# Optimization experiments

Hardware: AMD Instinct MI355X
Metric: run time of the kernel (lower is better)

## Reference

```python
import jax, jax.numpy as jnp
import numpy as np

N = 20000
E = 320000
H = 16
C = 16
NUM_GRAPHS = 64
NEG_SLOPE = 0.2


def _gat(x, edge_index, W, a_src, a_dst, bias):
    # PyG GATConv, concat=True, shared lin for src/dst, eval mode (no dropout)
    h = (x @ W).reshape(-1, H, C)                       # [N,H,C]
    src, dst = edge_index[0], edge_index[1]
    alpha_src = jnp.sum(h * a_src, axis=-1)             # [N,H]
    alpha_dst = jnp.sum(h * a_dst, axis=-1)             # [N,H]
    alpha = alpha_src[src] + alpha_dst[dst]             # [E,H]
    alpha = jax.nn.leaky_relu(alpha, NEG_SLOPE)
    amax = jax.ops.segment_max(alpha, dst, num_segments=N)
    ex = jnp.exp(alpha - amax[dst])
    denom = jax.ops.segment_sum(ex, dst, num_segments=N)
    attn = ex / jnp.where(denom == 0, 1.0, denom)[dst]  # [E,H]
    msg = h[src] * attn[:, :, None]                     # [E,H,C]
    out = jax.ops.segment_sum(msg, dst, num_segments=N) # [N,H,C]
    return out.reshape(-1, H * C) + bias


def setup_inputs() -> dict:
    key = jax.random.key(0)
    ks = jax.random.split(key, 32)
    d = {}
    d['x'] = jax.random.normal(ks[0], (N, 20), dtype=jnp.float32)
    d['edge_index_ipv6'] = jax.random.randint(ks[1], (2, E), 0, N)
    d['edge_attr_ipv6'] = jax.random.normal(ks[2], (E, 19), dtype=jnp.float32)
    d['edge_index_tsch'] = jax.random.randint(ks[3], (2, E), 0, N)
    d['edge_attr_tsch'] = jax.random.normal(ks[4], (E, 7), dtype=jnp.float32)
    d['batch'] = jnp.sort(jax.random.randint(ks[5], (N,), 0, NUM_GRAPHS))
    s = 0.1
    d['W_i'] = jax.random.normal(ks[6], (20, H * C), dtype=jnp.float32) * s
    d['a_src_i'] = jax.random.normal(ks[7], (H, C), dtype=jnp.float32) * s
    d['a_dst_i'] = jax.random.normal(ks[8], (H, C), dtype=jnp.float32) * s
    d['b_i'] = jnp.zeros((H * C,), dtype=jnp.float32)
    d['W_t'] = jax.random.normal(ks[9], (20, H * C), dtype=jnp.float32) * s
    d['a_src_t'] = jax.random.normal(ks[10], (H, C), dtype=jnp.float32) * s
    d['a_dst_t'] = jax.random.normal(ks[11], (H, C), dtype=jnp.float32) * s
    d['b_t'] = jnp.zeros((H * C,), dtype=jnp.float32)
    d['Wf'] = jax.random.normal(ks[12], (512, 64), dtype=jnp.float32) * s
    d['bf'] = jnp.zeros((64,), dtype=jnp.float32)
    d['W1'] = jax.random.normal(ks[13], (64, 32), dtype=jnp.float32) * s
    d['b1'] = jnp.zeros((32,), dtype=jnp.float32)
    d['W2'] = jax.random.normal(ks[14], (32, 16), dtype=jnp.float32) * s
    d['b2'] = jnp.zeros((16,), dtype=jnp.float32)
    d['W3'] = jax.random.normal(ks[15], (16, 16), dtype=jnp.float32) * s
    d['b3'] = jnp.zeros((16,), dtype=jnp.float32)
    d['Wce'] = jax.random.normal(ks[16], (16, 3), dtype=jnp.float32) * s
    d['bce'] = jnp.zeros((3,), dtype=jnp.float32)
    d['Wcv'] = jax.random.normal(ks[17], (16, 3), dtype=jnp.float32) * s
    d['bcv'] = jnp.zeros((3,), dtype=jnp.float32)
    return d


def reference(x, edge_index_ipv6, edge_attr_ipv6, edge_index_tsch, edge_attr_tsch,
              batch, W_i, a_src_i, a_dst_i, b_i, W_t, a_src_t, a_dst_t, b_t,
              Wf, bf, W1, b1, W2, b2, W3, b3, Wce, bce, Wcv, bcv):
    # edge_attr_* are ignored by GATConv (edge_dim=None in PyG), as in original
    n_ipv6 = _gat(x, edge_index_ipv6, W_i, a_src_i, a_dst_i, b_i)
    n_tsch = _gat(x, edge_index_tsch, W_t, a_src_t, a_dst_t, b_t)
    h = jnp.concatenate([n_ipv6, n_tsch], axis=-1)      # [N,512]
    h = jax.nn.relu(h @ Wf + bf)
    h = jax.nn.relu(h @ W1 + b1)
    h = jax.nn.relu(h @ W2 + b2)
    h = jax.nn.relu(h @ W3 + b3)                        # [N,16]
    ssum = jax.ops.segment_sum(h, batch, num_segments=NUM_GRAPHS)
    cnt = jax.ops.segment_sum(jnp.ones((h.shape[0], 1), h.dtype), batch,
                              num_segments=NUM_GRAPHS)
    g = ssum / jnp.where(cnt == 0, 1.0, cnt)            # [G,16]
    out_event = g @ Wce + bce
    out_env = g @ Wcv + bcv
    return out_event, out_env
```

## Files before the change

### kernel.cpp

```cpp
#include <hip/hip_runtime.h>
#include <math.h>

#define N_NODES 20000
#define N_EDGES 320000
#define NG 64
#define NEG 0.2f
#define NCHUNK ((N_NODES + 255) / 256)
#define FLAGBIT (1 << 30)

typedef __attribute__((ext_vector_type(8))) short bf16x8;
typedef __attribute__((ext_vector_type(4))) float f32x4;

__device__ __forceinline__ unsigned short f2bf(float f) {
  unsigned int u = __float_as_uint(f);
  return (unsigned short)((u + 0x7fffu + ((u >> 16) & 1u)) >> 16);
}

__global__ __launch_bounds__(256) void k_prep(
    const float* __restrict__ W_i, const float* __restrict__ as_i, const float* __restrict__ ad_i,
    const float* __restrict__ W_t, const float* __restrict__ as_t, const float* __restrict__ ad_t,
    const float* __restrict__ Wf, const float* __restrict__ bf,
    const float* __restrict__ b_i, const float* __restrict__ b_t,
    float* __restrict__ wsall, unsigned short* __restrict__ wbigfrag,
    float* __restrict__ bfold,
    int* __restrict__ fill_i, int* __restrict__ fill_t,
    float* __restrict__ gsum, int* __restrict__ gcnt, int* __restrict__ aggs) {
  __shared__ float bred[4][64];
  int idx = blockIdx.x * 256 + threadIdx.x;
  if (idx < 1280) {
    int k = idx >> 6, c = idx & 63;
    int set = c >> 5, role = (c >> 4) & 1, h = c & 15;
    const float* W = set ? W_t : W_i;
    const float* a = set ? (role ? ad_t : as_t) : (role ? ad_i : as_i);
    float v = 0.f;
#pragma unroll
    for (int j = 0; j < 16; ++j) v = fmaf(W[k * 256 + h * 16 + j], a[h * 16 + j], v);
    wsall[idx] = v;
    return;
  }
  idx -= 1280;
  if (idx < 49152) {
    int ct = idx / 12288, rem = idx % 12288;
    int lane = (rem >> 3) & 63, j = rem & 7, ks = rem >> 9;
    int k = ks * 32 + ((lane >> 4) << 3) + j;
    int nc = ct * 16 + (lane & 15);
    float v = 0.f;
    int g = (k >= 384) ? 1 : 0;
    int r = k - g * 384;
    int h = r / 24, c = r - h * 24;
    if (c < 20) {
      const float* W = g ? W_t : W_i;
      const float* wr = W + c * 256 + (h << 4);
      const float* wf = Wf + ((g << 8) + (h << 4)) * 64 + nc;
#pragma unroll
      for (int m = 0; m < 16; ++m) v = fmaf(wr[m], wf[m * 64], v);
    }
    wbigfrag[idx] = f2bf(v);
    return;
  }
  idx -= 49152;
  if (idx < 256) {
    int t = threadIdx.x, wv = t >> 6, j = t & 63;
    float p = 0.f;
    int i0 = wv * 128;
#pragma unroll 4
    for (int i = i0; i < i0 + 128; ++i) {
      float b = (i < 256) ? b_i[i] : b_t[i - 256];
      p = fmaf(b, Wf[i * 64 + j], p);
    }
    bred[wv][j] = p;
    __syncthreads();
    if (wv == 0) bfold[j] = bred[0][j] + bred[1][j] + bred[2][j] + bred[3][j] + bf[j];
    return;
  }
  idx -= 256;
  if (idx < N_NODES) { fill_i[idx] = 0; return; }
  idx -= N_NODES;
  if (idx < N_NODES) { fill_t[idx] = 0; return; }
  idx -= N_NODES;
  if (idx < NG * 16) { gsum[idx] = 0.f; return; }
  idx -= NG * 16;
  if (idx < NG) { gcnt[idx] = 0; return; }
  idx -= NG;
  if (idx < 256) aggs[idx] = 0;
}

__global__ __launch_bounds__(256) void k_alpha(
    const float* __restrict__ x, const float* __restrict__ wsall,
    float* __restrict__ xpad,
    float* __restrict__ asrc0, float* __restrict__ adst0,
    float* __restrict__ asrc1, float* __restrict__ adst1) {
  int t = threadIdx.x;
  int n0 = blockIdx.x * 16;
  __shared__ float xs[16][20];
  __shared__ float ws[20][64];
  for (int i = t; i < 16 * 20; i += 256) {
    int nd = i / 20, k = i % 20;
    xs[nd][k] = x[(n0 + nd) * 20 + k];
  }
  for (int i = t; i < 1280; i += 256) ws[i >> 6][i & 63] = wsall[i];
  __syncthreads();
  for (int i = t; i < 512; i += 256) {
    int nd = i >> 5, j = i & 31;
    xpad[(size_t)(n0 + nd) * 32 + j] = (j < 20) ? xs[nd][j] : 0.f;
  }
#pragma unroll
  for (int i = 0; i < 4; ++i) {
    int wi = i * 256 + t;
    int nd = wi >> 6, c = wi & 63;
    float v = 0.f;
#pragma unroll
    for (int k = 0; k < 20; ++k) v = fmaf(xs[nd][k], ws[k][c], v);
    int n = n0 + nd, h = c & 15;
    float* arr = (c >> 5) ? ((c >> 4) & 1 ? adst1 : asrc1)
                          : ((c >> 4) & 1 ? adst0 : asrc0);
    arr[n * 16 + h] = v;
  }
}

__global__ void k_hist(const int* __restrict__ ei0, const int* __restrict__ ei1,
                       int* __restrict__ cnt0, int* __restrict__ cnt1) {
  int e = blockIdx.x * blockDim.x + threadIdx.x;
  if (e >= N_EDGES) return;
  if (blockIdx.y == 0)
    atomicAdd(&cnt0[ei0[N_EDGES + e]], 1);
  else
    atomicAdd(&cnt1[ei1[N_EDGES + e]], 1);
}

__global__ __launch_bounds__(256) void k_scan(
    int* __restrict__ fill0, int* __restrict__ fill1,
    int* __restrict__ rp0, int* __restrict__ rp1,
    int* __restrict__ aggs) {
  int chunk = blockIdx.x, set = blockIdx.y;
  int* fill = set ? fill1 : fill0;
  int* rp = set ? rp1 : rp0;
  int t = threadIdx.x, lane = t & 63, wv = t >> 6;
  int i = chunk * 256 + t;
  int v = (i < N_NODES) ? fill[i] : 0;
  int s = v;
#pragma unroll
  for (int d = 1; d < 64; d <<= 1) {
    int o = __shfl_up(s, d);
    if (lane >= d) s += o;
  }
  __shared__ int wsum[4];
  if (lane == 63) wsum[wv] = s;
  __syncthreads();
  int pre = 0;
#pragma unroll
  for (int j = 0; j < 4; ++j)
    if (j < wv) pre += wsum[j];
  s += pre;
  int agg = wsum[0] + wsum[1] + wsum[2] + wsum[3];
  if (t == 0)
    __hip_atomic_store(&aggs[set * 128 + chunk], agg | FLAGBIT,
                       __ATOMIC_RELEASE, __HIP_MEMORY_SCOPE_AGENT);
  __shared__ int reds[256];
  int part = 0;
  for (int j = t; j < chunk; j += 256) {
    int a;
    do {
      a = __hip_atomic_load(&aggs[set * 128 + j], __ATOMIC_ACQUIRE,
                            __HIP_MEMORY_SCOPE_AGENT);
    } while (!(a & FLAGBIT));
    part += a & (FLAGBIT - 1);
  }
  reds[t] = part;
  __syncthreads();
  for (int st = 128; st > 0; st >>= 1) {
    if (t < st) reds[t] += reds[t + st];
    __syncthreads();
  }
  int carry = reds[0];
  int excl = carry + s - v;
  if (i < N_NODES) {
    rp[i] = excl;
    fill[i] = excl;
    if (i == N_NODES - 1) rp[N_NODES] = excl + v;
  }
}

__global__ void k_scatter(const int* __restrict__ ei0, const int* __restrict__ ei1,
                          int* __restrict__ fill0, int* __restrict__ fill1,
                          unsigned short* __restrict__ srcs0,
                          unsigned short* __restrict__ srcs1) {
  int e = blockIdx.x * blockDim.x + threadIdx.x;
  if (e >= N_EDGES) return;
  const int* ei = blockIdx.y ? ei1 : ei0;
  int* fill = blockIdx.y ? fill1 : fill0;
  unsigned short* srcs = blockIdx.y ? srcs1 : srcs0;
  int d = ei[N_EDGES + e];
  int pos = atomicAdd(&fill[d], 1);
  srcs[pos] = (unsigned short)ei[e];
}

__global__ __launch_bounds__(256) void k_gat(
    const float* __restrict__ xpad,
    const float* __restrict__ asrc0, const float* __restrict__ adst0,
    const float* __restrict__ asrc1, const float* __restrict__ adst1,
    const int* __restrict__ rp0, const unsigned short* __restrict__ srcs0,
    const int* __restrict__ rp1, const unsigned short* __restrict__ srcs1,
    unsigned short* __restrict__ xagg) {
  __shared__ float xsh[4][16][36];
  __shared__ float lath[4][16][16];
  int w4 = threadIdx.x >> 6, lane = threadIdx.x & 63;
  int n = blockIdx.x * 2 + (w4 >> 1);
  int g = w4 & 1;
  int h16 = lane & 15, e4 = lane >> 4;
  int eid = lane & 15, slot = lane >> 4;
  float (*xs)[36] = xsh[w4];
  float (*la)[16] = lath[w4];
  const float* asrc = g ? asrc1 : asrc0;
  const float* adst = g ? adst1 : adst0;
  const int* rp = g ? rp1 : rp0;
  const unsigned short* srcs = g ? srcs1 : srcs0;
  int k0 = rp[n], k1 = rp[n + 1];
  float4 adn4 = *(const float4*)&adst[n * 16 + slot * 4];
  float lacc = 0.f;
  float xa[8];
#pragma unroll
  for (int j = 0; j < 8; ++j) xa[j] = 0.f;
  if (k1 > k0) {
    int nbat = (k1 - k0 + 15) >> 4;
    int sb = (int)srcs[min(k0 + eid, k1 - 1)];
    float4 xv0 = *(const float4*)&xpad[(size_t)sb * 32 + slot * 8];
    float4 xv1 = *(const float4*)&xpad[(size_t)sb * 32 + slot * 8 + 4];
    float4 av4 = *(const float4*)&asrc[(size_t)sb * 16 + slot * 4];
    int sbN = 0;
    if (nbat > 1) sbN = (int)srcs[min(k0 + 16 + eid, k1 - 1)];
    for (int bb = 0; bb < nbat; ++bb) {
      float4 xv0N = {0.f,0.f,0.f,0.f}, xv1N = xv0N, av4N = xv0N;
      int sbNN = 0;
      if (bb + 1 < nbat) {
        xv0N = *(const float4*)&xpad[(size_t)sbN * 32 + slot * 8];
        xv1N = *(const float4*)&xpad[(size_t)sbN * 32 + slot * 8 + 4];
        av4N = *(const float4*)&asrc[(size_t)sbN * 16 + slot * 4];
      }
      if (bb + 2 < nbat)
        sbNN = (int)srcs[min(k0 + (bb + 2) * 16 + eid, k1 - 1)];
      bool val = (k0 + bb * 16 + eid) < k1;
      float4 ex4;
      {
        float a;
        a = av4.x + adn4.x; a = a >= 0.f ? a : NEG * a; ex4.x = val ? __expf(a) : 0.f;
        a = av4.y + adn4.y; a = a >= 0.f ? a : NEG * a; ex4.y = val ? __expf(a) : 0.f;
        a = av4.z + adn4.z; a = a >= 0.f ? a : NEG * a; ex4.z = val ? __expf(a) : 0.f;
        a = av4.w + adn4.w; a = a >= 0.f ? a : NEG * a; ex4.w = val ? __expf(a) : 0.f;
      }
      *(float4*)&xs[eid][slot * 8] = xv0;
      *(float4*)&xs[eid][slot * 8 + 4] = xv1;
      *(float4*)&la[eid][slot * 4] = ex4;
#pragma unroll
      for (int e = 0; e < 16; ++e) {
        float w = la[e][h16];
        lacc += w;
        float4 x0 = *(const float4*)&xs[e][e4 * 8];
        float4 x1 = *(const float4*)&xs[e][e4 * 8 + 4];
        xa[0] = fmaf(w, x0.x, xa[0]); xa[1] = fmaf(w, x0.y, xa[1]);
        xa[2] = fmaf(w, x0.z, xa[2]); xa[3] = fmaf(w, x0.w, xa[3]);
        xa[4] = fmaf(w, x1.x, xa[4]); xa[5] = fmaf(w, x1.y, xa[5]);
        xa[6] = fmaf(w, x1.z, xa[6]); xa[7] = fmaf(w, x1.w, xa[7]);
      }
      xv0 = xv0N; xv1 = xv1N; av4 = av4N; sb = sbN; sbN = sbNN;
    }
  }
  float invl = lacc > 0.f ? 1.f / lacc : 0.f;
  if (e4 < 3) {
    unsigned int u[4];
#pragma unroll
    for (int q = 0; q < 4; ++q)
      u[q] = (unsigned int)f2bf(xa[2 * q] * invl) |
             ((unsigned int)f2bf(xa[2 * q + 1] * invl) << 16);
    *(uint4*)&xagg[(size_t)n * 768 + g * 384 + h16 * 24 + e4 * 8] = *(uint4*)u;
  }
}

__global__ __launch_bounds__(256) void k_mlp(
    const unsigned short* __restrict__ xagg, const unsigned short* __restrict__ wbigfrag,
    const float* __restrict__ bfold,
    const float* __restrict__ W1m, const float* __restrict__ b1v,
    const float* __restrict__ W2m, const float* __restrict__ b2v,
    const float* __restrict__ W3m, const float* __restrict__ b3v,
    const int* __restrict__ batch,
    float* __restrict__ gsum, int* __restrict__ gcnt) {
  int t = threadIdx.x, w = t >> 6, lane = t & 63;
  int n0 = blockIdx.x * 16;
  __shared__ float o1[16][68];
  __shared__ float o2[16][36];
  __shared__ float o3[16][20];
  __shared__ float o4[16][17];
  __shared__ int bs[16];
  if (t < 16) bs[t] = batch[n0 + t];

  {
    int m = lane & 15, kb = lane >> 4;
    const unsigned short* aptr = xagg + (size_t)(n0 + m) * 768 + kb * 8;
    const unsigned short* bbase = wbigfrag + (size_t)w * 12288 + lane * 8;
    f32x4 acc = {0.f, 0.f, 0.f, 0.f};
#pragma unroll 6
    for (int ks = 0; ks < 24; ++ks) {
      bf16x8 af = *(const bf16x8*)(aptr + ks * 32);
      bf16x8 bfr = *(const bf16x8*)(bbase + (size_t)ks * 512);
      acc = __builtin_amdgcn_mfma_f32_16x16x32_bf16(af, bfr, acc, 0, 0, 0);
    }
    int col = lane & 15, rg = lane >> 4;
#pragma unroll
    for (int r = 0; r < 4; ++r) {
      int row = rg * 4 + r;
      o1[row][w * 16 + col] = fmaxf(acc[r] + bfold[w * 16 + col], 0.f);
    }
  }
  __syncthreads();
  int nd = t >> 4, js = t & 15;
  {
    float a0 = b1v[js], a1 = b1v[js + 16];
#pragma unroll 8
    for (int k = 0; k < 64; ++k) {
      float hv = o1[nd][k];
      a0 = fmaf(hv, W1m[k * 32 + js], a0);
      a1 = fmaf(hv, W1m[k * 32 + js + 16], a1);
    }
    o2[nd][js] = fmaxf(a0, 0.f);
    o2[nd][js + 16] = fmaxf(a1, 0.f);
  }
  __syncthreads();
  {
    float a = b2v[js];
#pragma unroll
    for (int k = 0; k < 32; ++k) a = fmaf(o2[nd][k], W2m[k * 16 + js], a);
    o3[nd][js] = fmaxf(a, 0.f);
  }
  __syncthreads();
  {
    float a = b3v[js];
#pragma unroll
    for (int k = 0; k < 16; ++k) a = fmaf(o3[nd][k], W3m[k * 16 + js], a);
    o4[nd][js] = fmaxf(a, 0.f);
  }
  __syncthreads();
  if (t < 128) {
    int s = t >> 4, jx = t & 15;
    int b = bs[0] + s;
    if (b <= bs[15]) {
      float sum = 0.f; int c = 0;
#pragma unroll
      for (int ndd = 0; ndd < 16; ++ndd)
        if (bs[ndd] == b) { sum += o4[ndd][jx]; ++c; }
      if (c > 0) {
        atomicAdd(&gsum[b * 16 + jx], sum);
        if (jx == 0) atomicAdd(&gcnt[b], c);
      }
    }
  }
}

__global__ void k_head(const float* __restrict__ gsum, const int* __restrict__ gcnt,
                       const float* __restrict__ Wce, const float* __restrict__ bce,
                       const float* __restrict__ Wcv, const float* __restrict__ bcv,
                       float* __restrict__ out) {
  int t = threadIdx.x;
  if (t >= 384) return;
  int half = t / 192, idx = t % 192;
  int b = idx / 3, r = idx % 3;
  float cnt = (float)gcnt[b];
  float inv = cnt > 0.f ? 1.f / cnt : 1.f;
  const float* Wc = half ? Wcv : Wce;
  const float* bc = half ? bcv : bce;
  float v = bc[r];
#pragma unroll
  for (int j = 0; j < 16; ++j) v = fmaf(gsum[b * 16 + j] * inv, Wc[j * 3 + r], v);
  out[t] = v;
}

extern "C" void kernel_launch(void* const* d_in, const int* in_sizes, int n_in,
                              void* d_out, int out_size, void* d_ws, size_t ws_size,
                              hipStream_t stream) {
  const float* x = (const float*)d_in[0];
  const int* ei_i = (const int*)d_in[1];
  const int* ei_t = (const int*)d_in[3];
  const int* batch = (const int*)d_in[5];
  const float* W_i = (const float*)d_in[6];
  const float* as_i = (const float*)d_in[7];
  const float* ad_i = (const float*)d_in[8];
  const float* b_i = (const float*)d_in[9];
  const float* W_t = (const float*)d_in[10];
  const float* as_t = (const float*)d_in[11];
  const float* ad_t = (const float*)d_in[12];
  const float* b_t = (const float*)d_in[13];
  const float* Wf = (const float*)d_in[14];
  const float* bf = (const float*)d_in[15];
  const float* W1 = (const float*)d_in[16];
  const float* b1 = (const float*)d_in[17];
  const float* W2 = (const float*)d_in[18];
  const float* b2 = (const float*)d_in[19];
  const float* W3 = (const float*)d_in[20];
  const float* b3 = (const float*)d_in[21];
  const float* Wce = (const float*)d_in[22];
  const float* bce = (const float*)d_in[23];
  const float* Wcv = (const float*)d_in[24];
  const float* bcv = (const float*)d_in[25];

  char* ws = (char*)d_ws;
  size_t off = 0;
  auto take = [&](size_t bytes) {
    void* p = ws + off;
    off = (off + bytes + 255) & ~(size_t)255;
    return p;
  };
  float* xpad = (float*)take((size_t)N_NODES * 32 * 4);
  unsigned short* xagg = (unsigned short*)take((size_t)N_NODES * 768 * 2);
  float* wsall = (float*)take((size_t)1280 * 4);
  unsigned short* wbigfrag = (unsigned short*)take((size_t)49152 * 2);
  float* bfold = (float*)take((size_t)64 * 4);
  float* asrc_i = (float*)take((size_t)N_NODES * 16 * 4);
  float* adst_i = (float*)take((size_t)N_NODES * 16 * 4);
  float* asrc_t = (float*)take((size_t)N_NODES * 16 * 4);
  float* adst_t = (float*)take((size_t)N_NODES * 16 * 4);
  int* rowptr_i = (int*)take((size_t)(N_NODES + 1) * 4);
  int* rowptr_t = (int*)take((size_t)(N_NODES + 1) * 4);
  int* fill_i = (int*)take((size_t)N_NODES * 4);
  int* fill_t = (int*)take((size_t)N_NODES * 4);
  int* csums = (int*)take((size_t)2 * 128 * 4);
  unsigned short* srcs_i = (unsigned short*)take((size_t)N_EDGES * 2);
  unsigned short* srcs_t = (unsigned short*)take((size_t)N_EDGES * 2);
  float* gsum = (float*)take((size_t)NG * 16 * 4);
  int* gcnt = (int*)take((size_t)NG * 4);

  int prep_items = 1280 + 49152 + 256 + N_NODES + N_NODES + NG * 16 + NG + 256;
  k_prep<<<(prep_items + 255) / 256, 256, 0, stream>>>(
      W_i, as_i, ad_i, W_t, as_t, ad_t, Wf, bf, b_i, b_t,
      wsall, wbigfrag, bfold, fill_i, fill_t, gsum, gcnt, csums);

  k_alpha<<<N_NODES / 16, 256, 0, stream>>>(x, wsall, xpad,
                                            asrc_i, adst_i, asrc_t, adst_t);

  dim3 egrid((N_EDGES + 255) / 256, 2);
  k_hist<<<egrid, 256, 0, stream>>>(ei_i, ei_t, fill_i, fill_t);
  dim3 sgrid(NCHUNK, 2);
  k_scan<<<sgrid, 256, 0, stream>>>(fill_i, fill_t, rowptr_i, rowptr_t, csums);
  k_scatter<<<egrid, 256, 0, stream>>>(ei_i, ei_t, fill_i, fill_t, srcs_i, srcs_t);

  k_gat<<<N_NODES / 2, 256, 0, stream>>>(xpad, asrc_i, adst_i, asrc_t, adst_t,
                                         rowptr_i, srcs_i, rowptr_t, srcs_t,
                                         xagg);

  k_mlp<<<N_NODES / 16, 256, 0, stream>>>(xagg, wbigfrag, bfold,
                                          W1, b1, W2, b2, W3, b3,
                                          batch, gsum, gcnt);

  k_head<<<1, 384, 0, stream>>>(gsum, gcnt, Wce, bce, Wcv, bcv, (float*)d_out);
}
```

Before: 165.1 us.

## Use bf16 MFMA for GAT neighbor aggregation with packed channel-major layout

The per-node GAT aggregation now runs on MFMA 16x16x32 bf16 instructions instead of scalar FMA loops through LDS, processing 32 edges per step. Node features are stored as bf16 with a constant-one channel at index 20, so the softmax denominator comes out of the same matrix product. The aggregated feature layout shrinks from 768 to 640 columns per node (channel-major, no per-head padding to 24), and the folded MLP weight fragments and the k_mlp loop shrink to match. This cuts gather bandwidth and ALU work, at the cost of bf16 rounding of the attention weights and features.

```diff
diff --git a/kernel.cpp b/kernel.cpp
--- a/kernel.cpp
+++ b/kernel.cpp
@@ -14,6 +14,9 @@
 __device__ __forceinline__ unsigned short f2bf(float f) {
   unsigned int u = __float_as_uint(f);
   return (unsigned short)((u + 0x7fffu + ((u >> 16) & 1u)) >> 16);
+}
+__device__ __forceinline__ unsigned int pk2bf(float a, float b) {
+  return (unsigned int)f2bf(a) | ((unsigned int)f2bf(b) << 16);
 }
 
 __global__ __launch_bounds__(256) void k_prep(
@@ -39,18 +42,18 @@
     return;
   }
   idx -= 1280;
-  if (idx < 49152) {
-    int ct = idx / 12288, rem = idx % 12288;
+  if (idx < 40960) {
+    int ct = idx / 10240, rem = idx % 10240;
     int lane = (rem >> 3) & 63, j = rem & 7, ks = rem >> 9;
     int k = ks * 32 + ((lane >> 4) << 3) + j;
     int nc = ct * 16 + (lane & 15);
+    int g = (k >= 320) ? 1 : 0;
+    int r = k - g * 320;
+    int ch = r >> 4, h = r & 15;
     float v = 0.f;
-    int g = (k >= 384) ? 1 : 0;
-    int r = k - g * 384;
-    int h = r / 24, c = r - h * 24;
-    if (c < 20) {
+    if (ch < 20) {
       const float* W = g ? W_t : W_i;
-      const float* wr = W + c * 256 + (h << 4);
+      const float* wr = W + ch * 256 + (h << 4);
       const float* wf = Wf + ((g << 8) + (h << 4)) * 64 + nc;
 #pragma unroll
       for (int m = 0; m < 16; ++m) v = fmaf(wr[m], wf[m * 64], v);
@@ -58,7 +61,7 @@
     wbigfrag[idx] = f2bf(v);
     return;
   }
-  idx -= 49152;
+  idx -= 40960;
   if (idx < 256) {
     int t = threadIdx.x, wv = t >> 6, j = t & 63;
     float p = 0.f;
@@ -87,7 +90,7 @@
 
 __global__ __launch_bounds__(256) void k_alpha(
     const float* __restrict__ x, const float* __restrict__ wsall,
-    float* __restrict__ xpad,
+    unsigned short* __restrict__ xpadbf,
     float* __restrict__ asrc0, float* __restrict__ adst0,
     float* __restrict__ asrc1, float* __restrict__ adst1) {
   int t = threadIdx.x;
@@ -102,7 +105,8 @@
   __syncthreads();
   for (int i = t; i < 512; i += 256) {
     int nd = i >> 5, j = i & 31;
-    xpad[(size_t)(n0 + nd) * 32 + j] = (j < 20) ? xs[nd][j] : 0.f;
+    float v = (j < 20) ? xs[nd][j] : (j == 20 ? 1.f : 0.f);
+    xpadbf[(size_t)(n0 + nd) * 32 + j] = f2bf(v);
   }
 #pragma unroll
   for (int i = 0; i < 4; ++i) {
@@ -196,83 +200,84 @@
 }
 
 __global__ __launch_bounds__(256) void k_gat(
-    const float* __restrict__ xpad,
+    const unsigned short* __restrict__ xpadbf,
     const float* __restrict__ asrc0, const float* __restrict__ adst0,
     const float* __restrict__ asrc1, const float* __restrict__ adst1,
     const int* __restrict__ rp0, const unsigned short* __restrict__ srcs0,
     const int* __restrict__ rp1, const unsigned short* __restrict__ srcs1,
     unsigned short* __restrict__ xagg) {
-  __shared__ float xsh[4][16][36];
-  __shared__ float lath[4][16][16];
+  __shared__ unsigned short exsh[4][16][40];
+  __shared__ unsigned short xtsh[4][2][16][40];
   int w4 = threadIdx.x >> 6, lane = threadIdx.x & 63;
   int n = blockIdx.x * 2 + (w4 >> 1);
   int g = w4 & 1;
-  int h16 = lane & 15, e4 = lane >> 4;
   int eid = lane & 15, slot = lane >> 4;
-  float (*xs)[36] = xsh[w4];
-  float (*la)[16] = lath[w4];
+  unsigned short (*ext)[40] = exsh[w4];
+  unsigned short (*xtw)[16][40] = xtsh[w4];
   const float* asrc = g ? asrc1 : asrc0;
   const float* adst = g ? adst1 : adst0;
   const int* rp = g ? rp1 : rp0;
   const unsigned short* srcs = g ? srcs1 : srcs0;
   int k0 = rp[n], k1 = rp[n + 1];
-  float4 adn4 = *(const float4*)&adst[n * 16 + slot * 4];
-  float lacc = 0.f;
-  float xa[8];
-#pragma unroll
-  for (int j = 0; j < 8; ++j) xa[j] = 0.f;
-  if (k1 > k0) {
-    int nbat = (k1 - k0 + 15) >> 4;
-    int sb = (int)srcs[min(k0 + eid, k1 - 1)];
-    float4 xv0 = *(const float4*)&xpad[(size_t)sb * 32 + slot * 8];
-    float4 xv1 = *(const float4*)&xpad[(size_t)sb * 32 + slot * 8 + 4];
-    float4 av4 = *(const float4*)&asrc[(size_t)sb * 16 + slot * 4];
-    int sbN = 0;
-    if (nbat > 1) sbN = (int)srcs[min(k0 + 16 + eid, k1 - 1)];
-    for (int bb = 0; bb < nbat; ++bb) {
-      float4 xv0N = {0.f,0.f,0.f,0.f}, xv1N = xv0N, av4N = xv0N;
-      int sbNN = 0;
-      if (bb + 1 < nbat) {
-        xv0N = *(const float4*)&xpad[(size_t)sbN * 32 + slot * 8];
-        xv1N = *(const float4*)&xpad[(size_t)sbN * 32 + slot * 8 + 4];
-        av4N = *(const float4*)&asrc[(size_t)sbN * 16 + slot * 4];
-      }
-      if (bb + 2 < nbat)
-        sbNN = (int)srcs[min(k0 + (bb + 2) * 16 + eid, k1 - 1)];
-      bool val = (k0 + bb * 16 + eid) < k1;
-      float4 ex4;
-      {
-        float a;
-        a = av4.x + adn4.x; a = a >= 0.f ? a : NEG * a; ex4.x = val ? __expf(a) : 0.f;
-        a = av4.y + adn4.y; a = a >= 0.f ? a : NEG * a; ex4.y = val ? __expf(a) : 0.f;
-        a = av4.z + adn4.z; a = a >= 0.f ? a : NEG * a; ex4.z = val ? __expf(a) : 0.f;
-        a = av4.w + adn4.w; a = a >= 0.f ? a : NEG * a; ex4.w = val ? __expf(a) : 0.f;
-      }
-      *(float4*)&xs[eid][slot * 8] = xv0;
-      *(float4*)&xs[eid][slot * 8 + 4] = xv1;
-      *(float4*)&la[eid][slot * 4] = ex4;
-#pragma unroll
-      for (int e = 0; e < 16; ++e) {
-        float w = la[e][h16];
-        lacc += w;
-        float4 x0 = *(const float4*)&xs[e][e4 * 8];
-        float4 x1 = *(const float4*)&xs[e][e4 * 8 + 4];
-        xa[0] = fmaf(w, x0.x, xa[0]); xa[1] = fmaf(w, x0.y, xa[1]);
-        xa[2] = fmaf(w, x0.z, xa[2]); xa[3] = fmaf(w, x0.w, xa[3]);
-        xa[4] = fmaf(w, x1.x, xa[4]); xa[5] = fmaf(w, x1.y, xa[5]);
-        xa[6] = fmaf(w, x1.z, xa[6]); xa[7] = fmaf(w, x1.w, xa[7]);
-      }
-      xv0 = xv0N; xv1 = xv1N; av4 = av4N; sb = sbN; sbN = sbNN;
-    }
-  }
-  float invl = lacc > 0.f ? 1.f / lacc : 0.f;
-  if (e4 < 3) {
-    unsigned int u[4];
-#pragma unroll
-    for (int q = 0; q < 4; ++q)
-      u[q] = (unsigned int)f2bf(xa[2 * q] * invl) |
-             ((unsigned int)f2bf(xa[2 * q + 1] * invl) << 16);
-    *(uint4*)&xagg[(size_t)n * 768 + g * 384 + h16 * 24 + e4 * 8] = *(uint4*)u;
+  const float4 adn4 = *(const float4*)&adst[n * 16 + slot * 4];
+  f32x4 acc0 = {0.f, 0.f, 0.f, 0.f}, acc1 = acc0;
+  int h16 = lane & 15, e8 = (lane >> 4) * 8;
+  for (int base = k0; base < k1; base += 32) {
+    int e0 = base + 2 * eid, e1 = e0 + 1;
+    int sa = (int)srcs[min(e0, k1 - 1)];
+    int sbb = (int)srcs[min(e1, k1 - 1)];
+    const float4 ava = *(const float4*)&asrc[sa * 16 + slot * 4];
+    const float4 avb = *(const float4*)&asrc[sbb * 16 + slot * 4];
+    const uint4 xra = *(const uint4*)&xpadbf[(size_t)sa * 32 + slot * 8];
+    const uint4 xrb = *(const uint4*)&xpadbf[(size_t)sbb * 32 + slot * 8];
+    float ea[4], eb[4];
+    {
+      float a;
+      bool v0 = e0 < k1, v1 = e1 < k1;
+      a = ava.x + adn4.x; a = a >= 0.f ? a : NEG * a; ea[0] = v0 ? __expf(a) : 0.f;
+      a = ava.y + adn4.y; a = a >= 0.f ? a : NEG * a; ea[1] = v0 ? __expf(a) : 0.f;
+      a = ava.z + adn4.z; a = a >= 0.f ? a : NEG * a; ea[2] = v0 ? __expf(a) : 0.f;
+      a = ava.w + adn4.w; a = a >= 0.f ? a : NEG * a; ea[3] = v0 ? __expf(a) : 0.f;
+      a = avb.x + adn4.x; a = a >= 0.f ? a : NEG * a; eb[0] = v1 ? __expf(a) : 0.f;
+      a = avb.y + adn4.y; a = a >= 0.f ? a : NEG * a; eb[1] = v1 ? __expf(a) : 0.f;
+      a = avb.z + adn4.z; a = a >= 0.f ? a : NEG * a; eb[2] = v1 ? __expf(a) : 0.f;
+      a = avb.w + adn4.w; a = a >= 0.f ? a : NEG * a; eb[3] = v1 ? __expf(a) : 0.f;
+    }
+#pragma unroll
+    for (int r = 0; r < 4; ++r)
+      *(unsigned int*)&ext[slot * 4 + r][2 * eid] = pk2bf(ea[r], eb[r]);
+    unsigned int ua[4] = {xra.x, xra.y, xra.z, xra.w};
+    unsigned int ub[4] = {xrb.x, xrb.y, xrb.z, xrb.w};
+#pragma unroll
+    for (int q = 0; q < 8; ++q) {
+      unsigned int baq = (q & 1) ? (ua[q >> 1] >> 16) : (ua[q >> 1] & 0xffffu);
+      unsigned int bbq = (q & 1) ? (ub[q >> 1] >> 16) : (ub[q >> 1] & 0xffffu);
+      int ch = slot * 8 + q;
+      *(unsigned int*)&xtw[ch >> 4][ch & 15][2 * eid] = baq | (bbq << 16);
+    }
+    bf16x8 A = *(const bf16x8*)&ext[h16][e8];
+    bf16x8 B0 = *(const bf16x8*)&xtw[0][h16][e8];
+    bf16x8 B1 = *(const bf16x8*)&xtw[1][h16][e8];
+    acc0 = __builtin_amdgcn_mfma_f32_16x16x32_bf16(A, B0, acc0, 0, 0, 0);
+    acc1 = __builtin_amdgcn_mfma_f32_16x16x32_bf16(A, B1, acc1, 0, 0, 0);
+  }
+  float inv[4];
+#pragma unroll
+  for (int r = 0; r < 4; ++r) {
+    float dr = __shfl(acc1[r], (lane & 48) | 4);
+    inv[r] = dr > 0.f ? 1.f / dr : 0.f;
+  }
+  int s = lane >> 4, c = lane & 15;
+  size_t nb = (size_t)n * 640 + g * 320;
+  uint2 o0;
+  o0.x = pk2bf(acc0[0] * inv[0], acc0[1] * inv[1]);
+  o0.y = pk2bf(acc0[2] * inv[2], acc0[3] * inv[3]);
+  *(uint2*)&xagg[nb + c * 16 + s * 4] = o0;
+  if (c < 4) {
+    uint2 o1;
+    o1.x = pk2bf(acc1[0] * inv[0], acc1[1] * inv[1]);
+    o1.y = pk2bf(acc1[2] * inv[2], acc1[3] * inv[3]);
+    *(uint2*)&xagg[nb + 256 + c * 16 + s * 4] = o1;
   }
 }
 
@@ -295,11 +300,11 @@
 
   {
     int m = lane & 15, kb = lane >> 4;
-    const unsigned short* aptr = xagg + (size_t)(n0 + m) * 768 + kb * 8;
-    const unsigned short* bbase = wbigfrag + (size_t)w * 12288 + lane * 8;
+    const unsigned short* aptr = xagg + (size_t)(n0 + m) * 640 + kb * 8;
+    const unsigned short* bbase = wbigfrag + (size_t)w * 10240 + lane * 8;
     f32x4 acc = {0.f, 0.f, 0.f, 0.f};
-#pragma unroll 6
-    for (int ks = 0; ks < 24; ++ks) {
+#pragma unroll 5
+    for (int ks = 0; ks < 20; ++ks) {
       bf16x8 af = *(const bf16x8*)(aptr + ks * 32);
       bf16x8 bfr = *(const bf16x8*)(bbase + (size_t)ks * 512);
       acc = __builtin_amdgcn_mfma_f32_16x16x32_bf16(af, bfr, acc, 0, 0, 0);
@@ -408,10 +413,10 @@
     off = (off + bytes + 255) & ~(size_t)255;
     return p;
   };
-  float* xpad = (float*)take((size_t)N_NODES * 32 * 4);
-  unsigned short* xagg = (unsigned short*)take((size_t)N_NODES * 768 * 2);
+  unsigned short* xpadbf = (unsigned short*)take((size_t)N_NODES * 32 * 2);
+  unsigned short* xagg = (unsigned short*)take((size_t)N_NODES * 640 * 2);
   float* wsall = (float*)take((size_t)1280 * 4);
-  unsigned short* wbigfrag = (unsigned short*)take((size_t)49152 * 2);
+  unsigned short* wbigfrag = (unsigned short*)take((size_t)40960 * 2);
   float* bfold = (float*)take((size_t)64 * 4);
   float* asrc_i = (float*)take((size_t)N_NODES * 16 * 4);
   float* adst_i = (float*)take((size_t)N_NODES * 16 * 4);
@@ -427,12 +432,12 @@
   float* gsum = (float*)take((size_t)NG * 16 * 4);
   int* gcnt = (int*)take((size_t)NG * 4);
 
-  int prep_items = 1280 + 49152 + 256 + N_NODES + N_NODES + NG * 16 + NG + 256;
+  int prep_items = 1280 + 40960 + 256 + N_NODES + N_NODES + NG * 16 + NG + 256;
   k_prep<<<(prep_items + 255) / 256, 256, 0, stream>>>(
       W_i, as_i, ad_i, W_t, as_t, ad_t, Wf, bf, b_i, b_t,
       wsall, wbigfrag, bfold, fill_i, fill_t, gsum, gcnt, csums);
 
-  k_alpha<<<N_NODES / 16, 256, 0, stream>>>(x, wsall, xpad,
+  k_alpha<<<N_NODES / 16, 256, 0, stream>>>(x, wsall, xpadbf,
                                             asrc_i, adst_i, asrc_t, adst_t);
 
   dim3 egrid((N_EDGES + 255) / 256, 2);
@@ -441,7 +446,7 @@
   k_scan<<<sgrid, 256, 0, stream>>>(fill_i, fill_t, rowptr_i, rowptr_t, csums);
   k_scatter<<<egrid, 256, 0, stream>>>(ei_i, ei_t, fill_i, fill_t, srcs_i, srcs_t);
 
-  k_gat<<<N_NODES / 2, 256, 0, stream>>>(xpad, asrc_i, adst_i, asrc_t, adst_t,
+  k_gat<<<N_NODES / 2, 256, 0, stream>>>(xpadbf, asrc_i, adst_i, asrc_t, adst_t,
                                          rowptr_i, srcs_i, rowptr_t, srcs_t,
                                          xagg);
 
```

Measured after the change: 136.8 us. 1.21x faster.
